# Kernel optimization log

Hardware: AMD Instinct MI355X
Metric: run time of the kernel (lower is better)

Reference implementation:

```python
import jax, jax.numpy as jnp
import numpy as np

N_NODES = 50000
N_EDGES = 800000
D_FEAT = 64
H = 128


def scatter_mean(x, idx, num_segments):
    # mean of x rows per segment; empty segments -> 0 (matches torch_scatter scatter_mean)
    s = jax.ops.segment_sum(x, idx, num_segments=num_segments)
    c = jax.ops.segment_sum(jnp.ones((x.shape[0],), dtype=x.dtype), idx, num_segments=num_segments)
    return s / jnp.maximum(c, 1.0)[:, None]


def setup_inputs() -> dict:
    key = jax.random.key(0)
    ks = jax.random.split(key, 6)
    edge_attr = jax.random.normal(ks[0], (N_EDGES, D_FEAT), dtype=jnp.float32)
    edge_index = jax.random.randint(ks[1], (2, N_EDGES), 0, N_NODES, dtype=jnp.int64 if jax.config.jax_enable_x64 else jnp.int32)
    # ensure max index == N_NODES - 1 so num_nodes inference matches
    edge_index = edge_index.at[0, 0].set(N_NODES - 1)
    sc = 0.05
    W0 = jax.random.normal(ks[2], (D_FEAT + D_FEAT, H), dtype=jnp.float32) * sc
    b0 = jnp.zeros((H,), dtype=jnp.float32)
    W1 = jax.random.normal(ks[3], (H + D_FEAT, H), dtype=jnp.float32) * sc
    b1 = jnp.zeros((H,), dtype=jnp.float32)
    Wf = jax.random.normal(ks[4], (2 * H, 1), dtype=jnp.float32) * sc
    bf = jnp.zeros((1,), dtype=jnp.float32)
    return {"edge_attr": edge_attr, "edge_index": edge_index,
            "W0": W0, "b0": b0, "W1": W1, "b1": b1, "Wf": Wf, "bf": bf}


def reference(edge_attr, edge_index, W0, b0, W1, b1, Wf, bf):
    src = edge_index[0]
    dst = edge_index[1]
    # initial node features: mean of incoming edge_attr over edge_index[1]
    node_attr = scatter_mean(edge_attr, dst, N_NODES)            # [N, D_FEAT]
    # layer 0: aggregate over edge_index[0], concat, linear, sigmoid
    agg = scatter_mean(edge_attr, src, N_NODES)                  # [N, D_FEAT]
    node_attr = jax.nn.sigmoid(jnp.concatenate([node_attr, agg], axis=1) @ W0 + b0)  # [N, H]
    # layer 1
    agg = scatter_mean(edge_attr, src, N_NODES)                  # [N, D_FEAT]
    node_attr = jax.nn.sigmoid(jnp.concatenate([node_attr, agg], axis=1) @ W1 + b1)  # [N, H]
    # final edge classifier: gather endpoints, concat, linear
    edge_embs = jnp.concatenate([node_attr[src], node_attr[dst]], axis=1)  # [E, 2H]
    embeddings = jax.lax.stop_gradient(edge_embs)
    logits = (edge_embs @ Wf + bf).reshape(-1)                   # [E]
    return logits, embeddings
```

## Files before the change

### kernel.cpp

```cpp
#include <hip/hip_runtime.h>
#include <hip/hip_bf16.h>

#define N_NODES 50000
#define N_EDGES 800000
#define D_FEAT 64
#define H 128
#define CAP 96

typedef float f32x4 __attribute__((ext_vector_type(4)));
typedef float f32x2 __attribute__((ext_vector_type(2)));

__global__ void k_fill(const int* __restrict__ ei,
                       int* __restrict__ cnt_dst, int* __restrict__ cnt_src,
                       int* __restrict__ bkt_dst, int* __restrict__ bkt_src) {
    int t = blockIdx.x * blockDim.x + threadIdx.x;
    if (t >= N_EDGES / 4) return;
    int4 s = ((const int4*)ei)[t];
    int4 d = ((const int4*)(ei + N_EDGES))[t];
    int e = 4 * t;
    int p;
    p = atomicAdd(&cnt_src[s.x], 1); if (p < CAP) bkt_src[(size_t)s.x * CAP + p] = e;
    p = atomicAdd(&cnt_src[s.y], 1); if (p < CAP) bkt_src[(size_t)s.y * CAP + p] = e + 1;
    p = atomicAdd(&cnt_src[s.z], 1); if (p < CAP) bkt_src[(size_t)s.z * CAP + p] = e + 2;
    p = atomicAdd(&cnt_src[s.w], 1); if (p < CAP) bkt_src[(size_t)s.w * CAP + p] = e + 3;
    p = atomicAdd(&cnt_dst[d.x], 1); if (p < CAP) bkt_dst[(size_t)d.x * CAP + p] = e;
    p = atomicAdd(&cnt_dst[d.y], 1); if (p < CAP) bkt_dst[(size_t)d.y * CAP + p] = e + 1;
    p = atomicAdd(&cnt_dst[d.z], 1); if (p < CAP) bkt_dst[(size_t)d.z * CAP + p] = e + 2;
    p = atomicAdd(&cnt_dst[d.w], 1); if (p < CAP) bkt_dst[(size_t)d.w * CAP + p] = e + 3;
}

__global__ __launch_bounds__(128) void k_node(const float* __restrict__ ea,
        const int* __restrict__ cnt_dst, const int* __restrict__ bkt_dst,
        const int* __restrict__ cnt_src, const int* __restrict__ bkt_src,
        const float* __restrict__ W0, const float* __restrict__ b0,
        const float* __restrict__ W1, const float* __restrict__ b1,
        const float* __restrict__ Wf,
        float* __restrict__ emb, float* __restrict__ ps, float* __restrict__ pd) {
    __shared__ float x0[16][128];
    __shared__ float x1[16][128];
    __shared__ float red[16][2][2];
    __shared__ int ccnt[32];
    int t = threadIdx.x;
    int n0 = blockIdx.x * 16;

    {
        int unit = t >> 2;
        int l = t & 3;
        int nn = unit >> 1;
        int dir = unit & 1;
        int n = n0 + nn;
        const int* cnt = dir ? cnt_src : cnt_dst;
        const int* bkt = dir ? bkt_src : bkt_dst;
        int c = cnt[n];
        int cc = c < CAP ? c : CAP;
        size_t b = (size_t)n * CAP;
        f32x4 a0 = {0.f,0.f,0.f,0.f}, a1 = {0.f,0.f,0.f,0.f};
        f32x4 a2 = {0.f,0.f,0.f,0.f}, a3 = {0.f,0.f,0.f,0.f};
        int i = 0;
        for (; i + 2 <= cc; i += 2) {
            int e0 = bkt[b + i];
            int e1 = bkt[b + i + 1];
            const float* r0 = ea + (size_t)e0 * D_FEAT;
            const float* r1 = ea + (size_t)e1 * D_FEAT;
            f32x4 u0 = *(const f32x4*)(r0 + 4 * l);
            f32x4 u1 = *(const f32x4*)(r0 + 4 * l + 16);
            f32x4 u2 = *(const f32x4*)(r0 + 4 * l + 32);
            f32x4 u3 = *(const f32x4*)(r0 + 4 * l + 48);
            f32x4 w0 = *(const f32x4*)(r1 + 4 * l);
            f32x4 w1 = *(const f32x4*)(r1 + 4 * l + 16);
            f32x4 w2 = *(const f32x4*)(r1 + 4 * l + 32);
            f32x4 w3 = *(const f32x4*)(r1 + 4 * l + 48);
            a0 += u0; a1 += u1; a2 += u2; a3 += u3;
            a0 += w0; a1 += w1; a2 += w2; a3 += w3;
        }
        if (i < cc) {
            int e0 = bkt[b + i];
            const float* r0 = ea + (size_t)e0 * D_FEAT;
            a0 += *(const f32x4*)(r0 + 4 * l);
            a1 += *(const f32x4*)(r0 + 4 * l + 16);
            a2 += *(const f32x4*)(r0 + 4 * l + 32);
            a3 += *(const f32x4*)(r0 + 4 * l + 48);
        }
        float dinv = 1.0f / fmaxf((float)c, 1.0f);
        a0 *= dinv; a1 *= dinv; a2 *= dinv; a3 *= dinv;
        float* xr = &x0[nn][dir * 64 + 4 * l];
        *(f32x4*)(xr)      = a0;
        *(f32x4*)(xr + 16) = a1;
        *(f32x4*)(xr + 32) = a2;
        *(f32x4*)(xr + 48) = a3;
        if (l == 0) ccnt[unit] = cc;
    }
    __syncthreads();
    {
        float acc[16];
        float bias = b0[t];
        #pragma unroll
        for (int n = 0; n < 16; n++) acc[n] = bias;
        for (int k = 0; k < 128; k += 4) {
            float w0 = W0[(k + 0) * 128 + t];
            float w1 = W0[(k + 1) * 128 + t];
            float w2 = W0[(k + 2) * 128 + t];
            float w3 = W0[(k + 3) * 128 + t];
            #pragma unroll
            for (int n = 0; n < 16; n++) {
                f32x4 xv = *(const f32x4*)&x0[n][k];
                acc[n] = fmaf(xv.x, w0, acc[n]);
                acc[n] = fmaf(xv.y, w1, acc[n]);
                acc[n] = fmaf(xv.z, w2, acc[n]);
                acc[n] = fmaf(xv.w, w3, acc[n]);
            }
        }
        #pragma unroll
        for (int n = 0; n < 16; n++) x1[n][t] = 1.0f / (1.0f + __expf(-acc[n]));
    }
    __syncthreads();
    float hv[16];
    {
        float acc[16];
        float bias = b1[t];
        #pragma unroll
        for (int n = 0; n < 16; n++) acc[n] = bias;
        for (int k = 0; k < 128; k += 4) {
            float w0 = W1[(k + 0) * 128 + t];
            float w1 = W1[(k + 1) * 128 + t];
            float w2 = W1[(k + 2) * 128 + t];
            float w3 = W1[(k + 3) * 128 + t];
            #pragma unroll
            for (int n = 0; n < 16; n++) {
                f32x4 xv = *(const f32x4*)&x1[n][k];
                acc[n] = fmaf(xv.x, w0, acc[n]);
                acc[n] = fmaf(xv.y, w1, acc[n]);
                acc[n] = fmaf(xv.z, w2, acc[n]);
                acc[n] = fmaf(xv.w, w3, acc[n]);
            }
        }
        for (int k = 128; k < 192; k += 4) {
            float w0 = W1[(k + 0) * 128 + t];
            float w1 = W1[(k + 1) * 128 + t];
            float w2 = W1[(k + 2) * 128 + t];
            float w3 = W1[(k + 3) * 128 + t];
            #pragma unroll
            for (int n = 0; n < 16; n++) {
                f32x4 xv = *(const f32x4*)&x0[n][k - 64];
                acc[n] = fmaf(xv.x, w0, acc[n]);
                acc[n] = fmaf(xv.y, w1, acc[n]);
                acc[n] = fmaf(xv.z, w2, acc[n]);
                acc[n] = fmaf(xv.w, w3, acc[n]);
            }
        }
        #pragma unroll
        for (int n = 0; n < 16; n++) hv[n] = 1.0f / (1.0f + __expf(-acc[n]));
    }
    {
        float wlo = Wf[t];
        float whi = Wf[128 + t];
        int wv = t >> 6, ln = t & 63;
        #pragma unroll
        for (int n = 0; n < 16; n++) {
            float a = hv[n] * wlo;
            float b = hv[n] * whi;
            #pragma unroll
            for (int off = 32; off > 0; off >>= 1) {
                a += __shfl_xor(a, off, 64);
                b += __shfl_xor(b, off, 64);
            }
            if (ln == 0) { red[n][0][wv] = a; red[n][1][wv] = b; }
        }
    }
    __syncthreads();
    float (*h1s)[128] = x0;
    #pragma unroll
    for (int n = 0; n < 16; n++) h1s[n][t] = hv[n];
    if (t < 32) {
        int n = t >> 1, half = t & 1;
        float v = red[n][half][0] + red[n][half][1];
        if (half == 0) ps[n0 + n] = v; else pd[n0 + n] = v;
    }
    __syncthreads();
    {
        int wv = t >> 6;
        int lane = t & 63;
        int j = lane >> 5;
        int q = lane & 31;
        for (int Li = 0; Li < 16; Li++) {
            int L = wv * 16 + Li;
            int nn = L >> 1;
            int dir = L & 1;
            int half = 1 - dir;
            const int* bl = (dir ? bkt_src : bkt_dst) + (size_t)(n0 + nn) * CAP;
            int c = ccnt[L];
            f32x4 hreg = *(const f32x4*)&h1s[nn][q * 4];
            size_t boff = (size_t)half * 128 + q * 4;
            int i = j;
            for (; i + 2 < c; i += 4) {
                int e0 = bl[i];
                int e1 = bl[i + 2];
                __builtin_nontemporal_store(hreg, (f32x4*)(emb + (size_t)e0 * 256 + boff));
                __builtin_nontemporal_store(hreg, (f32x4*)(emb + (size_t)e1 * 256 + boff));
            }
            for (; i < c; i += 2) {
                int e0 = bl[i];
                __builtin_nontemporal_store(hreg, (f32x4*)(emb + (size_t)e0 * 256 + boff));
            }
        }
    }
}

__global__ void k_logits(const int* __restrict__ ei, const float* __restrict__ ps,
                         const float* __restrict__ pd, const float* __restrict__ bfp,
                         float* __restrict__ logits) {
    int t = blockIdx.x * blockDim.x + threadIdx.x;
    if (t >= N_EDGES / 2) return;
    int2 s = ((const int2*)ei)[t];
    int2 d = ((const int2*)(ei + N_EDGES))[t];
    float b = bfp[0];
    f32x2 r = { ps[s.x] + pd[d.x] + b, ps[s.y] + pd[d.y] + b };
    __builtin_nontemporal_store(r, (f32x2*)logits + t);
}

extern "C" void kernel_launch(void* const* d_in, const int* in_sizes, int n_in,
                              void* d_out, int out_size, void* d_ws, size_t ws_size,
                              hipStream_t stream) {
    const float* edge_attr  = (const float*)d_in[0];
    const int*   edge_index = (const int*)d_in[1];
    const float* W0  = (const float*)d_in[2];
    const float* b0  = (const float*)d_in[3];
    const float* W1  = (const float*)d_in[4];
    const float* b1  = (const float*)d_in[5];
    const float* Wf  = (const float*)d_in[6];
    const float* bfp = (const float*)d_in[7];

    float* out = (float*)d_out;
    float* logits = out;
    float* emb    = out + N_EDGES;

    float* ws = (float*)d_ws;
    float* ps      = ws;
    float* pd      = ps + 50000;
    int*   cnt_dst = (int*)(pd + 50000);
    int*   cnt_src = cnt_dst + 50000;
    int*   bkt_dst = cnt_src + 50000;
    int*   bkt_src = bkt_dst + (size_t)N_NODES * CAP;

    hipMemsetAsync(cnt_dst, 0, 2 * N_NODES * sizeof(int), stream);

    {
        int grid = (N_EDGES / 4 + 255) / 256;
        k_fill<<<grid, 256, 0, stream>>>(edge_index, cnt_dst, cnt_src, bkt_dst, bkt_src);
    }
    {
        k_node<<<3125, 128, 0, stream>>>(edge_attr, cnt_dst, bkt_dst, cnt_src, bkt_src,
                                         W0, b0, W1, b1, Wf, emb, ps, pd);
    }
    {
        int grid = (N_EDGES / 2 + 255) / 256;
        k_logits<<<grid, 256, 0, stream>>>(edge_index, ps, pd, bfp, logits);
    }
}
```

Measured before the change: 408.1 us.

## Replace bucket-scatter embedding writes with per-edge gather from stored node features

The node kernel no longer scatters each node's hidden vector into the embedding rows of its incident edges. It now writes the hidden features to a workspace buffer. A new per-edge kernel, with one wavefront per edge, gathers the source and destination rows, writes the 256-float embedding row contiguously, and computes the logit. This trades scattered partial-row stores for coalesced full-row writes, at the cost of an extra 25.6MB write and a gathered read of node features. It also removes the dependency on capped buckets for the embedding output.

```diff
diff --git a/kernel.cpp b/kernel.cpp
--- a/kernel.cpp
+++ b/kernel.cpp
@@ -8,7 +8,6 @@
 #define CAP 96
 
 typedef float f32x4 __attribute__((ext_vector_type(4)));
-typedef float f32x2 __attribute__((ext_vector_type(2)));
 
 __global__ void k_fill(const int* __restrict__ ei,
                        int* __restrict__ cnt_dst, int* __restrict__ cnt_src,
@@ -35,11 +34,10 @@
         const float* __restrict__ W0, const float* __restrict__ b0,
         const float* __restrict__ W1, const float* __restrict__ b1,
         const float* __restrict__ Wf,
-        float* __restrict__ emb, float* __restrict__ ps, float* __restrict__ pd) {
+        float* __restrict__ h1, float* __restrict__ ps, float* __restrict__ pd) {
     __shared__ float x0[16][128];
     __shared__ float x1[16][128];
     __shared__ float red[16][2][2];
-    __shared__ int ccnt[32];
     int t = threadIdx.x;
     int n0 = blockIdx.x * 16;
 
@@ -88,7 +86,6 @@
         *(f32x4*)(xr + 16) = a1;
         *(f32x4*)(xr + 32) = a2;
         *(f32x4*)(xr + 48) = a3;
-        if (l == 0) ccnt[unit] = cc;
     }
     __syncthreads();
     {
@@ -151,6 +148,8 @@
         #pragma unroll
         for (int n = 0; n < 16; n++) hv[n] = 1.0f / (1.0f + __expf(-acc[n]));
     }
+    #pragma unroll
+    for (int n = 0; n < 16; n++) h1[(size_t)(n0 + n) * 128 + t] = hv[n];
     {
         float wlo = Wf[t];
         float whi = Wf[128 + t];
@@ -168,54 +167,28 @@
         }
     }
     __syncthreads();
-    float (*h1s)[128] = x0;
-    #pragma unroll
-    for (int n = 0; n < 16; n++) h1s[n][t] = hv[n];
     if (t < 32) {
         int n = t >> 1, half = t & 1;
         float v = red[n][half][0] + red[n][half][1];
         if (half == 0) ps[n0 + n] = v; else pd[n0 + n] = v;
     }
-    __syncthreads();
-    {
-        int wv = t >> 6;
-        int lane = t & 63;
-        int j = lane >> 5;
-        int q = lane & 31;
-        for (int Li = 0; Li < 16; Li++) {
-            int L = wv * 16 + Li;
-            int nn = L >> 1;
-            int dir = L & 1;
-            int half = 1 - dir;
-            const int* bl = (dir ? bkt_src : bkt_dst) + (size_t)(n0 + nn) * CAP;
-            int c = ccnt[L];
-            f32x4 hreg = *(const f32x4*)&h1s[nn][q * 4];
-            size_t boff = (size_t)half * 128 + q * 4;
-            int i = j;
-            for (; i + 2 < c; i += 4) {
-                int e0 = bl[i];
-                int e1 = bl[i + 2];
-                __builtin_nontemporal_store(hreg, (f32x4*)(emb + (size_t)e0 * 256 + boff));
-                __builtin_nontemporal_store(hreg, (f32x4*)(emb + (size_t)e1 * 256 + boff));
-            }
-            for (; i < c; i += 2) {
-                int e0 = bl[i];
-                __builtin_nontemporal_store(hreg, (f32x4*)(emb + (size_t)e0 * 256 + boff));
-            }
-        }
-    }
-}
-
-__global__ void k_logits(const int* __restrict__ ei, const float* __restrict__ ps,
-                         const float* __restrict__ pd, const float* __restrict__ bfp,
-                         float* __restrict__ logits) {
-    int t = blockIdx.x * blockDim.x + threadIdx.x;
-    if (t >= N_EDGES / 2) return;
-    int2 s = ((const int2*)ei)[t];
-    int2 d = ((const int2*)(ei + N_EDGES))[t];
-    float b = bfp[0];
-    f32x2 r = { ps[s.x] + pd[d.x] + b, ps[s.y] + pd[d.y] + b };
-    __builtin_nontemporal_store(r, (f32x2*)logits + t);
+}
+
+__global__ __launch_bounds__(256) void k_out(const int* __restrict__ ei,
+        const float* __restrict__ h1, const float* __restrict__ ps,
+        const float* __restrict__ pd, const float* __restrict__ bfp,
+        float* __restrict__ logits, float* __restrict__ emb) {
+    int gid = blockIdx.x * blockDim.x + threadIdx.x;
+    int e = gid >> 6;
+    int l = gid & 63;
+    if (e >= N_EDGES) return;
+    int src = ei[e];
+    int dst = ei[N_EDGES + e];
+    int node = (l < 32) ? src : dst;
+    f32x4 v = *(const f32x4*)(h1 + (size_t)node * 128 + (l & 31) * 4);
+    __builtin_nontemporal_store(v, (f32x4*)(emb + (size_t)e * 256 + l * 4));
+    if (l == 0)
+        __builtin_nontemporal_store(ps[src] + pd[dst] + bfp[0], &logits[e]);
 }
 
 extern "C" void kernel_launch(void* const* d_in, const int* in_sizes, int n_in,
@@ -235,7 +208,8 @@
     float* emb    = out + N_EDGES;
 
     float* ws = (float*)d_ws;
-    float* ps      = ws;
+    float* h1      = ws;
+    float* ps      = ws + 6400000;
     float* pd      = ps + 50000;
     int*   cnt_dst = (int*)(pd + 50000);
     int*   cnt_src = cnt_dst + 50000;
@@ -250,10 +224,11 @@
     }
     {
         k_node<<<3125, 128, 0, stream>>>(edge_attr, cnt_dst, bkt_dst, cnt_src, bkt_src,
-                                         W0, b0, W1, b1, Wf, emb, ps, pd);
-    }
-    {
-        int grid = (N_EDGES / 2 + 255) / 256;
-        k_logits<<<grid, 256, 0, stream>>>(edge_index, ps, pd, bfp, logits);
-    }
-}
+                                         W0, b0, W1, b1, Wf, h1, ps, pd);
+    }
+    {
+        long long total = (long long)N_EDGES * 64;
+        int grid = (int)((total + 255) / 256);
+        k_out<<<grid, 256, 0, stream>>>(edge_index, h1, ps, pd, bfp, logits, emb);
+    }
+}
```

After: 505.1 us. 1.24x slower.
